# Optimization experiments

Hardware: AMD Instinct MI355X
Metric: run time of the kernel (lower is better)

## Reference

```python
import jax
import jax.numpy as jnp
import numpy as np

NPOINT = 512
RADIUS = 0.2
K = 32


def setup_inputs() -> dict:
    key = jax.random.key(0)
    k1, k2 = jax.random.split(key)
    xyz = jax.random.uniform(k1, (8, 16384, 3), dtype=jnp.float32)      # [B,N,3] in unit cube
    features = jax.random.normal(k2, (8, 128, 16384), dtype=jnp.float32)  # [B,D,N]
    return {"xyz": xyz, "features": features}


def farthest_point_sample(xyz, npoint):
    # xyz: [B,N,3] -> centroids [B,npoint] int32. Deterministic start at index 0
    # (the torch code does randint(...)*0).
    B, N, _ = xyz.shape
    init_dist = jnp.full((B, N), 1e10, dtype=xyz.dtype)
    init_far = jnp.zeros((B,), dtype=jnp.int32)

    def step(carry, _):
        distance, farthest = carry
        centroid = jnp.take_along_axis(xyz, farthest[:, None, None], axis=1)  # [B,1,3]
        d = jnp.sum((xyz - centroid) ** 2, axis=-1)                           # [B,N]
        distance = jnp.minimum(distance, d)
        new_far = jnp.argmax(distance, axis=-1).astype(jnp.int32)
        return (distance, new_far), farthest

    (_, _), cents = jax.lax.scan(step, (init_dist, init_far), None, length=npoint)
    return cents.T  # [B, npoint]


def square_distance(src, dst):
    # src [B,S,3], dst [B,N,3] -> [B,S,N]
    d = -2.0 * jnp.einsum("bsc,bnc->bsn", src, dst)
    d = d + jnp.sum(src ** 2, -1)[:, :, None]
    d = d + jnp.sum(dst ** 2, -1)[:, None, :]
    return d


def query_ball_point(radius, nsample, xyz, new_xyz):
    B, N, _ = xyz.shape
    sqrd = square_distance(new_xyz, xyz)                              # [B,S,N]
    arangeN = jnp.arange(N, dtype=jnp.int32)[None, None, :]
    idx = jnp.where(sqrd > radius ** 2, N, arangeN)                   # out-of-ball -> sentinel N
    idx = jnp.sort(idx, axis=-1)[:, :, :nsample]                      # [B,S,K]
    first = idx[:, :, :1]
    idx = jnp.where(idx == N, first, idx)                             # pad with first valid neighbor
    return idx


def index_points(points, idx):
    # points [B,N,C], idx [B,...] -> [B,...,C]
    B = points.shape[0]
    bidx = jnp.arange(B).reshape((B,) + (1,) * (idx.ndim - 1))
    return points[bidx, idx]


def reference(xyz, features):
    # xyz [B,N,3], features [B,D,N]
    cent = farthest_point_sample(xyz, NPOINT)                 # [B,S]
    new_xyz = index_points(xyz, cent)                         # [B,S,3]
    idx = query_ball_point(RADIUS, K, xyz, new_xyz)           # [B,S,K]
    pts = jnp.transpose(features, (0, 2, 1))                  # [B,N,D]
    grouped = index_points(pts, idx)                          # [B,S,K,D]
    sub_features = jnp.max(grouped, axis=2)                   # [B,S,D]  (max over K neighbors)
    sub_features = jnp.transpose(sub_features, (0, 2, 1))     # [B,D,S]
    return new_xyz, sub_features
```

## Files before the change

### kernel.cpp

```cpp
#include <hip/hip_runtime.h>
#include <stdint.h>
#include <math.h>

#define NB      8
#define NPTS    16384
#define NPOINT  512
#define NCH     128
#define KNBR    32
#define R2      0.04f

#define DPP_ARG_STEP(v, p, CTRL) do {                                          \
    float _ov = __builtin_bit_cast(float, __builtin_amdgcn_update_dpp(         \
        __builtin_bit_cast(int, (v)), __builtin_bit_cast(int, (v)),            \
        (CTRL), 0xF, 0xF, false));                                             \
    int _op = __builtin_amdgcn_update_dpp((p), (p), (CTRL), 0xF, 0xF, false);  \
    bool _t = (_ov > (v)) || ((_ov == (v)) && (_op < (p)));                    \
    (v) = _t ? _ov : (v);                                                      \
    (p) = _t ? _op : (p);                                                      \
} while (0)

#define SHFL_ARG_STEP(v, p, XORAMT) do {                                       \
    float _ov = __shfl_xor((v), (XORAMT), 64);                                 \
    int   _op = __shfl_xor((p), (XORAMT), 64);                                 \
    bool _t = (_ov > (v)) || ((_ov == (v)) && (_op < (p)));                    \
    (v) = _t ? _ov : (v);                                                      \
    (p) = _t ? _op : (p);                                                      \
} while (0)

__global__
__attribute__((amdgpu_flat_work_group_size(1024, 1024)))
__attribute__((amdgpu_waves_per_eu(4, 4)))
void fps_transpose_kernel(const float* __restrict__ xyz,
                          const float* __restrict__ feat,
                          float* __restrict__ out,
                          int* __restrict__ cent,
                          float* __restrict__ ft,
                          int use_ft)
{
    const int blk = blockIdx.x;
    const int tid = threadIdx.x;

    if (blk < NB) {
        const int b = blk;
        const float* xb = xyz + (size_t)b * NPTS * 3;
        float px[16], py[16], pz[16], dist[16];
#pragma unroll
        for (int k = 0; k < 16; ++k) {
            int p = k * 1024 + tid;
            px[k] = xb[p * 3 + 0];
            py[k] = xb[p * 3 + 1];
            pz[k] = xb[p * 3 + 2];
            dist[k] = 1e10f;
        }
        __shared__ float s_v[16];
        __shared__ int   s_p[16];
        __shared__ float s_cx, s_cy, s_cz;
        const int lane = tid & 63;
        const int wid  = tid >> 6;

        if (tid == 0) {
            cent[b * NPOINT + 0] = 0;
            out[((size_t)b * NPOINT + 0) * 3 + 0] = xb[0];
            out[((size_t)b * NPOINT + 0) * 3 + 1] = xb[1];
            out[((size_t)b * NPOINT + 0) * 3 + 2] = xb[2];
            s_cx = xb[0]; s_cy = xb[1]; s_cz = xb[2];
        }
        __syncthreads();

        for (int i = 1; i < NPOINT; ++i) {
            const float cx = s_cx, cy = s_cy, cz = s_cz;
            float bv = -1.0f; int bk = 0;
#pragma unroll
            for (int k = 0; k < 16; ++k) {
                float dx = __fsub_rn(px[k], cx);
                float dy = __fsub_rn(py[k], cy);
                float dz = __fsub_rn(pz[k], cz);
                float d  = __fadd_rn(__fadd_rn(__fmul_rn(dx, dx),
                                               __fmul_rn(dy, dy)),
                                     __fmul_rn(dz, dz));
                float nd = fminf(dist[k], d);
                dist[k] = nd;
                if (nd > bv) { bv = nd; bk = k; }
            }
            float rv = bv;
            int   rp = bk * 1024 + tid;
            DPP_ARG_STEP(rv, rp, 0xB1);
            DPP_ARG_STEP(rv, rp, 0x4E);
            DPP_ARG_STEP(rv, rp, 0x141);
            DPP_ARG_STEP(rv, rp, 0x140);
            SHFL_ARG_STEP(rv, rp, 16);
            SHFL_ARG_STEP(rv, rp, 32);
            if (lane == 0) { s_v[wid] = rv; s_p[wid] = rp; }
            __syncthreads();
            float fv = s_v[lane & 15];
            int   fp = s_p[lane & 15];
            DPP_ARG_STEP(fv, fp, 0xB1);
            DPP_ARG_STEP(fv, fp, 0x4E);
            DPP_ARG_STEP(fv, fp, 0x141);
            DPP_ARG_STEP(fv, fp, 0x140);
            const int cur = __builtin_amdgcn_readfirstlane(fp);
            if (tid == (cur & 1023)) {
                const int kk = cur >> 10;
                float ox = 0.f, oy = 0.f, oz = 0.f;
#define CASE_K(K) case K: ox = px[K]; oy = py[K]; oz = pz[K]; break;
                switch (kk) {
                    CASE_K(0)  CASE_K(1)  CASE_K(2)  CASE_K(3)
                    CASE_K(4)  CASE_K(5)  CASE_K(6)  CASE_K(7)
                    CASE_K(8)  CASE_K(9)  CASE_K(10) CASE_K(11)
                    CASE_K(12) CASE_K(13) CASE_K(14) CASE_K(15)
                }
#undef CASE_K
                s_cx = ox; s_cy = oy; s_cz = oz;
                cent[b * NPOINT + i] = cur;
                size_t o = ((size_t)b * NPOINT + i) * 3;
                out[o + 0] = ox; out[o + 1] = oy; out[o + 2] = oz;
            }
            __syncthreads();
        }
    } else {
        if (!use_ft) return;
        int t  = blk - NB;
        int b  = t >> 11;
        int r  = t & 2047;
        int ct = r >> 9;
        int nt = r & 511;
        __shared__ float tile[32][33];
        int tx = tid & 31, ty = tid >> 5;
        int c = ct * 32 + ty, n = nt * 32 + tx;
        tile[ty][tx] = feat[((size_t)b * NCH + c) * NPTS + n];
        __syncthreads();
        int n2 = nt * 32 + ty, c2 = ct * 32 + tx;
        ft[((size_t)b * NPTS + n2) * NCH + c2] = tile[tx][ty];
    }
}

__global__ __launch_bounds__(256, 4)
void query_pool_kernel(const float* __restrict__ xyz,
                       const float* __restrict__ feat,
                       const float* __restrict__ ft,
                       const int* __restrict__ cent,
                       float* __restrict__ out_sub,
                       int use_ft)
{
    const int tid  = threadIdx.x;
    const int widx = tid >> 6;
    const int lane = tid & 63;
    const int w = blockIdx.x * 4 + widx;
    const int b = w >> 9;
    const int s = w & 511;

    const float* xb = xyz + (size_t)b * NPTS * 3;
    const int ci = cent[b * NPOINT + s];
    const float sx = xb[ci * 3 + 0];
    const float sy = xb[ci * 3 + 1];
    const float sz = xb[ci * 3 + 2];
    const float snorm = __fadd_rn(__fadd_rn(__fmul_rn(sx, sx),
                                            __fmul_rn(sy, sy)),
                                  __fmul_rn(sz, sz));

    __shared__ int lidx[4][KNBR];
    int found = 0;
    for (int base = 0; base < NPTS && found < KNBR; base += 64) {
        int j = base + lane;
        float dx = xb[j * 3 + 0];
        float dy = xb[j * 3 + 1];
        float dz = xb[j * 3 + 2];
        float dn = __fadd_rn(__fadd_rn(__fmul_rn(dx, dx),
                                       __fmul_rn(dy, dy)),
                             __fmul_rn(dz, dz));
        float dot = __fadd_rn(__fadd_rn(__fmul_rn(sx, dx),
                                        __fmul_rn(sy, dy)),
                              __fmul_rn(sz, dz));
        float d = __fadd_rn(__fadd_rn(__fmul_rn(-2.0f, dot), snorm), dn);
        bool inball = !(d > R2);
        unsigned long long mask = __ballot(inball);
        int before = (int)__popcll(mask & ((1ULL << lane) - 1ULL));
        int slot = found + before;
        if (inball && slot < KNBR) lidx[widx][slot] = j;
        found += (int)__popcll(mask);
    }
    int cnt = found < KNBR ? found : KNBR;
    __syncthreads();

    float a0 = -INFINITY, a1 = -INFINITY;
    if (use_ft) {
        for (int m = 0; m < cnt; ++m) {
            int i = lidx[widx][m];
            const float* row = ft + ((size_t)b * NPTS + i) * NCH;
            a0 = fmaxf(a0, row[lane]);
            a1 = fmaxf(a1, row[lane + 64]);
        }
    } else {
        for (int m = 0; m < cnt; ++m) {
            int i = lidx[widx][m];
            a0 = fmaxf(a0, feat[((size_t)b * NCH + lane) * NPTS + i]);
            a1 = fmaxf(a1, feat[((size_t)b * NCH + lane + 64) * NPTS + i]);
        }
    }
    out_sub[((size_t)b * NCH + lane) * NPOINT + s] = a0;
    out_sub[((size_t)b * NCH + lane + 64) * NPOINT + s] = a1;
}

extern "C" void kernel_launch(void* const* d_in, const int* in_sizes, int n_in,
                              void* d_out, int out_size, void* d_ws, size_t ws_size,
                              hipStream_t stream)
{
    const float* xyz  = (const float*)d_in[0];
    const float* feat = (const float*)d_in[1];
    float* out = (float*)d_out;

    int*   cent = (int*)d_ws;
    float* ft   = (float*)((char*)d_ws + 16384);
    const size_t need_ft = 16384ull + (size_t)NB * NPTS * NCH * 4ull;
    int use_ft = (ws_size >= need_ft) ? 1 : 0;

    int nblocks1 = use_ft ? (NB + NB * (NCH / 32) * (NPTS / 32)) : NB;
    hipLaunchKernelGGL(fps_transpose_kernel, dim3(nblocks1), dim3(1024), 0, stream,
                       xyz, feat, out, cent, ft, use_ft);

    hipLaunchKernelGGL(query_pool_kernel, dim3((NB * NPOINT) / 4), dim3(256), 0, stream,
                       xyz, feat, ft, cent, out + (size_t)NB * NPOINT * 3, use_ft);
}
```

Measured before the change: 1.170 ms.

## Pack FPS distance math, drop second barrier via double-buffered reduction and global centroid reload

The farthest-point-sampling loop now holds point coordinates as float2 pairs and computes distances with packed v_pk_add/v_pk_mul instructions. Each thread fetches the next centroid from global memory (a uniform scalar load) instead of having the owning thread broadcast it through shared memory. Double-buffering the per-wave reduction slots lets the second __syncthreads per iteration be removed. This cuts one barrier and the select switch from each of the 511 serial iterations, at the cost of a dependent global load per iteration on the critical path. Distances are now computed as p + (-c), which is exactly equal to p - c, so results stay bit-identical.

```diff
diff --git a/kernel.cpp b/kernel.cpp
--- a/kernel.cpp
+++ b/kernel.cpp
@@ -8,6 +8,19 @@
 #define NCH     128
 #define KNBR    32
 #define R2      0.04f
+
+typedef float v2f __attribute__((ext_vector_type(2)));
+
+__device__ __forceinline__ v2f pk_add(v2f a, v2f b) {
+    v2f d;
+    asm("v_pk_add_f32 %0, %1, %2" : "=v"(d) : "v"(a), "v"(b));
+    return d;
+}
+__device__ __forceinline__ v2f pk_mul(v2f a, v2f b) {
+    v2f d;
+    asm("v_pk_mul_f32 %0, %1, %2" : "=v"(d) : "v"(a), "v"(b));
+    return d;
+}
 
 #define DPP_ARG_STEP(v, p, CTRL) do {                                          \
     float _ov = __builtin_bit_cast(float, __builtin_amdgcn_update_dpp(         \
@@ -43,44 +56,48 @@
     if (blk < NB) {
         const int b = blk;
         const float* xb = xyz + (size_t)b * NPTS * 3;
-        float px[16], py[16], pz[16], dist[16];
+        v2f px[8], py[8], pz[8], dist[8];
 #pragma unroll
-        for (int k = 0; k < 16; ++k) {
-            int p = k * 1024 + tid;
-            px[k] = xb[p * 3 + 0];
-            py[k] = xb[p * 3 + 1];
-            pz[k] = xb[p * 3 + 2];
-            dist[k] = 1e10f;
-        }
-        __shared__ float s_v[16];
-        __shared__ int   s_p[16];
-        __shared__ float s_cx, s_cy, s_cz;
+        for (int j = 0; j < 8; ++j) {
+            int p0 = (2 * j) * 1024 + tid;
+            int p1 = p0 + 1024;
+            px[j] = (v2f){xb[p0 * 3 + 0], xb[p1 * 3 + 0]};
+            py[j] = (v2f){xb[p0 * 3 + 1], xb[p1 * 3 + 1]};
+            pz[j] = (v2f){xb[p0 * 3 + 2], xb[p1 * 3 + 2]};
+            dist[j] = (v2f){1e10f, 1e10f};
+        }
+        __shared__ float s_v[2][16];
+        __shared__ int   s_p[2][16];
         const int lane = tid & 63;
         const int wid  = tid >> 6;
 
+        int   cur = 0;
+        float cx = xb[0], cy = xb[1], cz = xb[2];
         if (tid == 0) {
             cent[b * NPOINT + 0] = 0;
-            out[((size_t)b * NPOINT + 0) * 3 + 0] = xb[0];
-            out[((size_t)b * NPOINT + 0) * 3 + 1] = xb[1];
-            out[((size_t)b * NPOINT + 0) * 3 + 2] = xb[2];
-            s_cx = xb[0]; s_cy = xb[1]; s_cz = xb[2];
-        }
-        __syncthreads();
+            out[((size_t)b * NPOINT + 0) * 3 + 0] = cx;
+            out[((size_t)b * NPOINT + 0) * 3 + 1] = cy;
+            out[((size_t)b * NPOINT + 0) * 3 + 2] = cz;
+        }
 
         for (int i = 1; i < NPOINT; ++i) {
-            const float cx = s_cx, cy = s_cy, cz = s_cz;
+            v2f ncx = (v2f){-cx, -cx};
+            v2f ncy = (v2f){-cy, -cy};
+            v2f ncz = (v2f){-cz, -cz};
             float bv = -1.0f; int bk = 0;
 #pragma unroll
-            for (int k = 0; k < 16; ++k) {
-                float dx = __fsub_rn(px[k], cx);
-                float dy = __fsub_rn(py[k], cy);
-                float dz = __fsub_rn(pz[k], cz);
-                float d  = __fadd_rn(__fadd_rn(__fmul_rn(dx, dx),
-                                               __fmul_rn(dy, dy)),
-                                     __fmul_rn(dz, dz));
-                float nd = fminf(dist[k], d);
-                dist[k] = nd;
-                if (nd > bv) { bv = nd; bk = k; }
+            for (int j = 0; j < 8; ++j) {
+                v2f dx = pk_add(px[j], ncx);
+                v2f dy = pk_add(py[j], ncy);
+                v2f dz = pk_add(pz[j], ncz);
+                v2f s  = pk_add(pk_add(pk_mul(dx, dx), pk_mul(dy, dy)),
+                                pk_mul(dz, dz));
+                float nd0 = fminf(dist[j].x, s.x);
+                float nd1 = fminf(dist[j].y, s.y);
+                dist[j].x = nd0; dist[j].y = nd1;
+                float pv = fmaxf(nd0, nd1);
+                int   pi = (nd1 > nd0) ? (2 * j + 1) : (2 * j);
+                if (pv > bv) { bv = pv; bk = pi; }
             }
             float rv = bv;
             int   rp = bk * 1024 + tid;
@@ -90,32 +107,24 @@
             DPP_ARG_STEP(rv, rp, 0x140);
             SHFL_ARG_STEP(rv, rp, 16);
             SHFL_ARG_STEP(rv, rp, 32);
-            if (lane == 0) { s_v[wid] = rv; s_p[wid] = rp; }
+            const int buf = i & 1;
+            if (lane == 0) { s_v[buf][wid] = rv; s_p[buf][wid] = rp; }
             __syncthreads();
-            float fv = s_v[lane & 15];
-            int   fp = s_p[lane & 15];
+            float fv = s_v[buf][lane & 15];
+            int   fp = s_p[buf][lane & 15];
             DPP_ARG_STEP(fv, fp, 0xB1);
             DPP_ARG_STEP(fv, fp, 0x4E);
             DPP_ARG_STEP(fv, fp, 0x141);
             DPP_ARG_STEP(fv, fp, 0x140);
-            const int cur = __builtin_amdgcn_readfirstlane(fp);
-            if (tid == (cur & 1023)) {
-                const int kk = cur >> 10;
-                float ox = 0.f, oy = 0.f, oz = 0.f;
-#define CASE_K(K) case K: ox = px[K]; oy = py[K]; oz = pz[K]; break;
-                switch (kk) {
-                    CASE_K(0)  CASE_K(1)  CASE_K(2)  CASE_K(3)
-                    CASE_K(4)  CASE_K(5)  CASE_K(6)  CASE_K(7)
-                    CASE_K(8)  CASE_K(9)  CASE_K(10) CASE_K(11)
-                    CASE_K(12) CASE_K(13) CASE_K(14) CASE_K(15)
-                }
-#undef CASE_K
-                s_cx = ox; s_cy = oy; s_cz = oz;
+            cur = __builtin_amdgcn_readfirstlane(fp);
+            cx = xb[cur * 3 + 0];
+            cy = xb[cur * 3 + 1];
+            cz = xb[cur * 3 + 2];
+            if (tid == 0) {
                 cent[b * NPOINT + i] = cur;
                 size_t o = ((size_t)b * NPOINT + i) * 3;
-                out[o + 0] = ox; out[o + 1] = oy; out[o + 2] = oz;
+                out[o + 0] = cx; out[o + 1] = cy; out[o + 2] = cz;
             }
-            __syncthreads();
         }
     } else {
         if (!use_ft) return;
```

After: 1.288 ms. 10.1% more time.

## Split farthest-point sampling across 32 single-wave blocks with global-atomic argmax exchange

Applied to the files above, without the earlier changes.

Farthest-point sampling moves from one 1024-thread block per batch to 32 single-wave blocks per batch, so the work is spread over many CUs. Each step, every block publishes a packed (iteration tag, distance bits, inverted index) word to a double-buffered global slot array and spin-waits until all 32 peers have posted. The new centroid is then recovered with a shuffle max over the packed keys. This replaces block-wide barriers with agent-scope atomic polling, which needs all FPS blocks resident at once and may pay cross-XCD L2 latency on every iteration. The transpose blocks are also reshaped to 64 threads that each loop over rows.

```diff
diff --git a/kernel.cpp b/kernel.cpp
--- a/kernel.cpp
+++ b/kernel.cpp
@@ -8,6 +8,15 @@
 #define NCH     128
 #define KNBR    32
 #define R2      0.04f
+
+#define FPS_BPB   32
+#define FPS_NBLK  (NB * FPS_BPB)
+#define PPB       (NPTS / FPS_BPB)
+#define PPT       (PPB / 64)
+
+#define CENT_OFF   0
+#define SLOTS_OFF  16384
+#define FT_OFF     20480
 
 #define DPP_ARG_STEP(v, p, CTRL) do {                                          \
     float _ov = __builtin_bit_cast(float, __builtin_amdgcn_update_dpp(         \
@@ -28,109 +37,123 @@
 } while (0)
 
 __global__
-__attribute__((amdgpu_flat_work_group_size(1024, 1024)))
-__attribute__((amdgpu_waves_per_eu(4, 4)))
+__attribute__((amdgpu_flat_work_group_size(64, 64)))
 void fps_transpose_kernel(const float* __restrict__ xyz,
                           const float* __restrict__ feat,
                           float* __restrict__ out,
                           int* __restrict__ cent,
+                          unsigned long long* __restrict__ slots,
                           float* __restrict__ ft,
                           int use_ft)
 {
     const int blk = blockIdx.x;
     const int tid = threadIdx.x;
 
-    if (blk < NB) {
-        const int b = blk;
+    if (blk < FPS_NBLK) {
+        const int b = blk >> 5;
+        const int g = blk & 31;
         const float* xb = xyz + (size_t)b * NPTS * 3;
-        float px[16], py[16], pz[16], dist[16];
-#pragma unroll
-        for (int k = 0; k < 16; ++k) {
-            int p = k * 1024 + tid;
+        unsigned long long* sb = slots + b * 64;
+
+        float px[PPT], py[PPT], pz[PPT], d[PPT];
+#pragma unroll
+        for (int k = 0; k < PPT; ++k) {
+            int p = g * PPB + k * 64 + tid;
             px[k] = xb[p * 3 + 0];
             py[k] = xb[p * 3 + 1];
             pz[k] = xb[p * 3 + 2];
-            dist[k] = 1e10f;
-        }
-        __shared__ float s_v[16];
-        __shared__ int   s_p[16];
-        __shared__ float s_cx, s_cy, s_cz;
-        const int lane = tid & 63;
-        const int wid  = tid >> 6;
-
-        if (tid == 0) {
+            d[k] = 1e10f;
+        }
+        float cx = xb[0], cy = xb[1], cz = xb[2];
+        if (g == 0 && tid == 0) {
             cent[b * NPOINT + 0] = 0;
-            out[((size_t)b * NPOINT + 0) * 3 + 0] = xb[0];
-            out[((size_t)b * NPOINT + 0) * 3 + 1] = xb[1];
-            out[((size_t)b * NPOINT + 0) * 3 + 2] = xb[2];
-            s_cx = xb[0]; s_cy = xb[1]; s_cz = xb[2];
-        }
-        __syncthreads();
+            out[((size_t)b * NPOINT + 0) * 3 + 0] = cx;
+            out[((size_t)b * NPOINT + 0) * 3 + 1] = cy;
+            out[((size_t)b * NPOINT + 0) * 3 + 2] = cz;
+        }
 
         for (int i = 1; i < NPOINT; ++i) {
-            const float cx = s_cx, cy = s_cy, cz = s_cz;
-            float bv = -1.0f; int bk = 0;
-#pragma unroll
-            for (int k = 0; k < 16; ++k) {
+            float vmax = -1.0f;
+#pragma unroll
+            for (int k = 0; k < PPT; ++k) {
                 float dx = __fsub_rn(px[k], cx);
                 float dy = __fsub_rn(py[k], cy);
                 float dz = __fsub_rn(pz[k], cz);
-                float d  = __fadd_rn(__fadd_rn(__fmul_rn(dx, dx),
+                float dd = __fadd_rn(__fadd_rn(__fmul_rn(dx, dx),
                                                __fmul_rn(dy, dy)),
                                      __fmul_rn(dz, dz));
-                float nd = fminf(dist[k], d);
-                dist[k] = nd;
-                if (nd > bv) { bv = nd; bk = k; }
-            }
-            float rv = bv;
-            int   rp = bk * 1024 + tid;
+                float nd = fminf(d[k], dd);
+                d[k] = nd;
+                vmax = fmaxf(vmax, nd);
+            }
+            int bk = PPT - 1;
+#pragma unroll
+            for (int k = PPT - 2; k >= 0; --k) bk = (d[k] == vmax) ? k : bk;
+
+            float rv = vmax;
+            int   rp = g * PPB + bk * 64 + tid;
             DPP_ARG_STEP(rv, rp, 0xB1);
             DPP_ARG_STEP(rv, rp, 0x4E);
             DPP_ARG_STEP(rv, rp, 0x141);
             DPP_ARG_STEP(rv, rp, 0x140);
             SHFL_ARG_STEP(rv, rp, 16);
             SHFL_ARG_STEP(rv, rp, 32);
-            if (lane == 0) { s_v[wid] = rv; s_p[wid] = rp; }
-            __syncthreads();
-            float fv = s_v[lane & 15];
-            int   fp = s_p[lane & 15];
-            DPP_ARG_STEP(fv, fp, 0xB1);
-            DPP_ARG_STEP(fv, fp, 0x4E);
-            DPP_ARG_STEP(fv, fp, 0x141);
-            DPP_ARG_STEP(fv, fp, 0x140);
-            const int cur = __builtin_amdgcn_readfirstlane(fp);
-            if (tid == (cur & 1023)) {
-                const int kk = cur >> 10;
-                float ox = 0.f, oy = 0.f, oz = 0.f;
-#define CASE_K(K) case K: ox = px[K]; oy = py[K]; oz = pz[K]; break;
-                switch (kk) {
-                    CASE_K(0)  CASE_K(1)  CASE_K(2)  CASE_K(3)
-                    CASE_K(4)  CASE_K(5)  CASE_K(6)  CASE_K(7)
-                    CASE_K(8)  CASE_K(9)  CASE_K(10) CASE_K(11)
-                    CASE_K(12) CASE_K(13) CASE_K(14) CASE_K(15)
-                }
-#undef CASE_K
-                s_cx = ox; s_cy = oy; s_cz = oz;
-                cent[b * NPOINT + i] = cur;
+
+            const int parity = i & 1;
+            unsigned long long* sp = sb + parity * 32;
+            if (tid == 0) {
+                unsigned long long packed =
+                    ((unsigned long long)(unsigned)i << 48) |
+                    ((unsigned long long)__float_as_uint(rv) << 16) |
+                    (unsigned long long)(0xFFFFu ^ (unsigned)rp);
+                __hip_atomic_store(sp + g, packed, __ATOMIC_RELAXED,
+                                   __HIP_MEMORY_SCOPE_AGENT);
+            }
+            const unsigned long long itag = (unsigned long long)(unsigned)i;
+            unsigned long long q;
+            for (;;) {
+                q = __hip_atomic_load(sp + (tid & 31), __ATOMIC_RELAXED,
+                                      __HIP_MEMORY_SCOPE_AGENT);
+                if (__ballot((q >> 48) == itag) == ~0ULL) break;
+            }
+#pragma unroll
+            for (int s = 1; s <= 16; s <<= 1) {
+                unsigned long long o = __shfl_xor(q, s, 64);
+                q = (o > q) ? o : q;
+            }
+            unsigned widx = 0xFFFFu ^ (unsigned)(q & 0xFFFFull);
+            widx = __builtin_amdgcn_readfirstlane(widx);
+            cx = xb[widx * 3 + 0];
+            cy = xb[widx * 3 + 1];
+            cz = xb[widx * 3 + 2];
+            if (g == 0 && tid == 0) {
+                cent[b * NPOINT + i] = (int)widx;
                 size_t o = ((size_t)b * NPOINT + i) * 3;
-                out[o + 0] = ox; out[o + 1] = oy; out[o + 2] = oz;
-            }
-            __syncthreads();
+                out[o + 0] = cx; out[o + 1] = cy; out[o + 2] = cz;
+            }
         }
     } else {
         if (!use_ft) return;
-        int t  = blk - NB;
+        int t  = blk - FPS_NBLK;
         int b  = t >> 11;
         int r  = t & 2047;
         int ct = r >> 9;
         int nt = r & 511;
         __shared__ float tile[32][33];
-        int tx = tid & 31, ty = tid >> 5;
-        int c = ct * 32 + ty, n = nt * 32 + tx;
-        tile[ty][tx] = feat[((size_t)b * NCH + c) * NPTS + n];
+        int tx = tid & 31, ph = tid >> 5;
+#pragma unroll
+        for (int r2 = 0; r2 < 32; r2 += 2) {
+            int row = r2 + ph;
+            tile[row][tx] =
+                feat[((size_t)b * NCH + ct * 32 + row) * NPTS + nt * 32 + tx];
+        }
         __syncthreads();
-        int n2 = nt * 32 + ty, c2 = ct * 32 + tx;
-        ft[((size_t)b * NPTS + n2) * NCH + c2] = tile[tx][ty];
+#pragma unroll
+        for (int r2 = 0; r2 < 32; r2 += 2) {
+            int row = r2 + ph;
+            ft[((size_t)b * NPTS + nt * 32 + row) * NCH + ct * 32 + tx] =
+                tile[tx][row];
+        }
     }
 }
 
@@ -209,14 +232,17 @@
     const float* feat = (const float*)d_in[1];
     float* out = (float*)d_out;
 
-    int*   cent = (int*)d_ws;
-    float* ft   = (float*)((char*)d_ws + 16384);
-    const size_t need_ft = 16384ull + (size_t)NB * NPTS * NCH * 4ull;
+    int*   cent = (int*)((char*)d_ws + CENT_OFF);
+    unsigned long long* slots = (unsigned long long*)((char*)d_ws + SLOTS_OFF);
+    float* ft   = (float*)((char*)d_ws + FT_OFF);
+    const size_t need_ft = FT_OFF + (size_t)NB * NPTS * NCH * 4ull;
     int use_ft = (ws_size >= need_ft) ? 1 : 0;
 
-    int nblocks1 = use_ft ? (NB + NB * (NCH / 32) * (NPTS / 32)) : NB;
-    hipLaunchKernelGGL(fps_transpose_kernel, dim3(nblocks1), dim3(1024), 0, stream,
-                       xyz, feat, out, cent, ft, use_ft);
+    hipMemsetAsync((char*)d_ws + SLOTS_OFF, 0xFF, NB * 64 * 8, stream);
+
+    int nblocks1 = FPS_NBLK + (use_ft ? NB * (NCH / 32) * (NPTS / 32) : 0);
+    hipLaunchKernelGGL(fps_transpose_kernel, dim3(nblocks1), dim3(64), 0, stream,
+                       xyz, feat, out, cent, slots, ft, use_ft);
 
     hipLaunchKernelGGL(query_pool_kernel, dim3((NB * NPOINT) / 4), dim3(256), 0, stream,
                        xyz, feat, ft, cent, out + (size_t)NB * NPOINT * 3, use_ft);
```

Result: slower. 1.416 ms (+21.0%).

## Halve FPS block size, double-buffer reduction scratch, and reload centroid from global memory

Applied to the files above, without the earlier changes.

The farthest-point-sampling block drops from 1024 to 512 threads, each holding 32 points, and the per-thread argmax becomes a max pass followed by a lowest-index lookup. The second __syncthreads per iteration is removed: partial results go to parity double-buffered shared slots filled by each 16-lane group, and every thread reloads the new centroid coordinates from global memory using the reduced index instead of having one thread broadcast them through shared memory. The transpose blocks now use 512 threads that each copy two elements. This trades a barrier per iteration for one dependent global load on the serial critical path, plus more register pressure per thread.

```diff
diff --git a/kernel.cpp b/kernel.cpp
--- a/kernel.cpp
+++ b/kernel.cpp
@@ -8,6 +8,12 @@
 #define NCH     128
 #define KNBR    32
 #define R2      0.04f
+
+#define FPS_THR 512
+#define PPT     (NPTS / FPS_THR)
+
+#define CENT_OFF 0
+#define FT_OFF   16384
 
 #define DPP_ARG_STEP(v, p, CTRL) do {                                          \
     float _ov = __builtin_bit_cast(float, __builtin_amdgcn_update_dpp(         \
@@ -28,8 +34,8 @@
 } while (0)
 
 __global__
-__attribute__((amdgpu_flat_work_group_size(1024, 1024)))
-__attribute__((amdgpu_waves_per_eu(4, 4)))
+__attribute__((amdgpu_flat_work_group_size(FPS_THR, FPS_THR)))
+__attribute__((amdgpu_waves_per_eu(2, 4)))
 void fps_transpose_kernel(const float* __restrict__ xyz,
                           const float* __restrict__ feat,
                           float* __restrict__ out,
@@ -43,79 +49,75 @@
     if (blk < NB) {
         const int b = blk;
         const float* xb = xyz + (size_t)b * NPTS * 3;
-        float px[16], py[16], pz[16], dist[16];
+        float px[PPT], py[PPT], pz[PPT], d[PPT];
 #pragma unroll
-        for (int k = 0; k < 16; ++k) {
-            int p = k * 1024 + tid;
+        for (int k = 0; k < PPT; ++k) {
+            int p = k * FPS_THR + tid;
             px[k] = xb[p * 3 + 0];
             py[k] = xb[p * 3 + 1];
             pz[k] = xb[p * 3 + 2];
-            dist[k] = 1e10f;
-        }
-        __shared__ float s_v[16];
-        __shared__ int   s_p[16];
-        __shared__ float s_cx, s_cy, s_cz;
+            d[k] = 1e10f;
+        }
+        __shared__ float s_v[2][32];
+        __shared__ int   s_p[2][32];
         const int lane = tid & 63;
         const int wid  = tid >> 6;
 
+        float cx = xb[0], cy = xb[1], cz = xb[2];
         if (tid == 0) {
             cent[b * NPOINT + 0] = 0;
-            out[((size_t)b * NPOINT + 0) * 3 + 0] = xb[0];
-            out[((size_t)b * NPOINT + 0) * 3 + 1] = xb[1];
-            out[((size_t)b * NPOINT + 0) * 3 + 2] = xb[2];
-            s_cx = xb[0]; s_cy = xb[1]; s_cz = xb[2];
-        }
-        __syncthreads();
+            out[((size_t)b * NPOINT + 0) * 3 + 0] = cx;
+            out[((size_t)b * NPOINT + 0) * 3 + 1] = cy;
+            out[((size_t)b * NPOINT + 0) * 3 + 2] = cz;
+        }
 
         for (int i = 1; i < NPOINT; ++i) {
-            const float cx = s_cx, cy = s_cy, cz = s_cz;
-            float bv = -1.0f; int bk = 0;
+            float vmax = -1.0f;
 #pragma unroll
-            for (int k = 0; k < 16; ++k) {
+            for (int k = 0; k < PPT; ++k) {
                 float dx = __fsub_rn(px[k], cx);
                 float dy = __fsub_rn(py[k], cy);
                 float dz = __fsub_rn(pz[k], cz);
-                float d  = __fadd_rn(__fadd_rn(__fmul_rn(dx, dx),
+                float dd = __fadd_rn(__fadd_rn(__fmul_rn(dx, dx),
                                                __fmul_rn(dy, dy)),
                                      __fmul_rn(dz, dz));
-                float nd = fminf(dist[k], d);
-                dist[k] = nd;
-                if (nd > bv) { bv = nd; bk = k; }
+                float nd = fminf(d[k], dd);
+                d[k] = nd;
+                vmax = fmaxf(vmax, nd);
             }
-            float rv = bv;
-            int   rp = bk * 1024 + tid;
+            int bk = PPT - 1;
+#pragma unroll
+            for (int k = PPT - 2; k >= 0; --k) bk = (d[k] == vmax) ? k : bk;
+
+            float rv = vmax;
+            int   rp = bk * FPS_THR + tid;
             DPP_ARG_STEP(rv, rp, 0xB1);
             DPP_ARG_STEP(rv, rp, 0x4E);
             DPP_ARG_STEP(rv, rp, 0x141);
             DPP_ARG_STEP(rv, rp, 0x140);
-            SHFL_ARG_STEP(rv, rp, 16);
-            SHFL_ARG_STEP(rv, rp, 32);
-            if (lane == 0) { s_v[wid] = rv; s_p[wid] = rp; }
+            const int par = i & 1;
+            if ((lane & 15) == 0) {
+                int slot = wid * 4 + (lane >> 4);
+                s_v[par][slot] = rv;
+                s_p[par][slot] = rp;
+            }
             __syncthreads();
-            float fv = s_v[lane & 15];
-            int   fp = s_p[lane & 15];
+            float fv = s_v[par][lane & 31];
+            int   fp = s_p[par][lane & 31];
             DPP_ARG_STEP(fv, fp, 0xB1);
             DPP_ARG_STEP(fv, fp, 0x4E);
             DPP_ARG_STEP(fv, fp, 0x141);
             DPP_ARG_STEP(fv, fp, 0x140);
+            SHFL_ARG_STEP(fv, fp, 16);
             const int cur = __builtin_amdgcn_readfirstlane(fp);
-            if (tid == (cur & 1023)) {
-                const int kk = cur >> 10;
-                float ox = 0.f, oy = 0.f, oz = 0.f;
-#define CASE_K(K) case K: ox = px[K]; oy = py[K]; oz = pz[K]; break;
-                switch (kk) {
-                    CASE_K(0)  CASE_K(1)  CASE_K(2)  CASE_K(3)
-                    CASE_K(4)  CASE_K(5)  CASE_K(6)  CASE_K(7)
-                    CASE_K(8)  CASE_K(9)  CASE_K(10) CASE_K(11)
-                    CASE_K(12) CASE_K(13) CASE_K(14) CASE_K(15)
-                }
-#undef CASE_K
-                s_cx = ox; s_cy = oy; s_cz = oz;
+            cx = xb[cur * 3 + 0];
+            cy = xb[cur * 3 + 1];
+            cz = xb[cur * 3 + 2];
+            if (tid == 0) {
                 cent[b * NPOINT + i] = cur;
                 size_t o = ((size_t)b * NPOINT + i) * 3;
-                out[o + 0] = ox; out[o + 1] = oy; out[o + 2] = oz;
+                out[o + 0] = cx; out[o + 1] = cy; out[o + 2] = cz;
             }
-            __syncthreads();
         }
     } else {
         if (!use_ft) return;
@@ -126,11 +128,15 @@
         int nt = r & 511;
         __shared__ float tile[32][33];
         int tx = tid & 31, ty = tid >> 5;
-        int c = ct * 32 + ty, n = nt * 32 + tx;
-        tile[ty][tx] = feat[((size_t)b * NCH + c) * NPTS + n];
+        tile[ty][tx] =
+            feat[((size_t)b * NCH + ct * 32 + ty) * NPTS + nt * 32 + tx];
+        tile[ty + 16][tx] =
+            feat[((size_t)b * NCH + ct * 32 + ty + 16) * NPTS + nt * 32 + tx];
         __syncthreads();
-        int n2 = nt * 32 + ty, c2 = ct * 32 + tx;
-        ft[((size_t)b * NPTS + n2) * NCH + c2] = tile[tx][ty];
+        ft[((size_t)b * NPTS + nt * 32 + ty) * NCH + ct * 32 + tx] =
+            tile[tx][ty];
+        ft[((size_t)b * NPTS + nt * 32 + ty + 16) * NCH + ct * 32 + tx] =
+            tile[tx][ty + 16];
     }
 }
 
@@ -209,13 +215,13 @@
     const float* feat = (const float*)d_in[1];
     float* out = (float*)d_out;
 
-    int*   cent = (int*)d_ws;
-    float* ft   = (float*)((char*)d_ws + 16384);
-    const size_t need_ft = 16384ull + (size_t)NB * NPTS * NCH * 4ull;
+    int*   cent = (int*)((char*)d_ws + CENT_OFF);
+    float* ft   = (float*)((char*)d_ws + FT_OFF);
+    const size_t need_ft = FT_OFF + (size_t)NB * NPTS * NCH * 4ull;
     int use_ft = (ws_size >= need_ft) ? 1 : 0;
 
-    int nblocks1 = use_ft ? (NB + NB * (NCH / 32) * (NPTS / 32)) : NB;
-    hipLaunchKernelGGL(fps_transpose_kernel, dim3(nblocks1), dim3(1024), 0, stream,
+    int nblocks1 = NB + (use_ft ? NB * (NCH / 32) * (NPTS / 32) : 0);
+    hipLaunchKernelGGL(fps_transpose_kernel, dim3(nblocks1), dim3(FPS_THR), 0, stream,
                        xyz, feat, out, cent, ft, use_ft);
 
     hipLaunchKernelGGL(query_pool_kernel, dim3((NB * NPOINT) / 4), dim3(256), 0, stream,
```

After: 1.107 ms. -5.4%, faster.
